# Kernel tuning notes

Measured on AMD Instinct MI355X. Metric: run time of the kernel, lower is better.

The kernel has to match this reference:

```python
import jax, jax.numpy as jnp
import numpy as np

N_NODES = 50000
N_EDGES = 1600000
IN_FEATS = 32
HIDDEN = 64
OUT_FEAT = 64


def setup_inputs() -> dict:
    key = jax.random.key(0)
    ks = jax.random.split(key, 8)
    inputs = jax.random.normal(ks[0], (N_NODES, IN_FEATS), dtype=jnp.float32)
    edge_weights = jax.random.uniform(ks[1], (N_EDGES, 1), dtype=jnp.float32)
    src = jax.random.randint(ks[2], (N_EDGES,), 0, N_NODES, dtype=jnp.int32)
    dst = jax.random.randint(ks[3], (N_EDGES,), 0, N_NODES, dtype=jnp.int32)
    W1 = jax.random.normal(ks[4], (IN_FEATS, HIDDEN), dtype=jnp.float32) / np.sqrt(IN_FEATS)
    b1 = jnp.zeros((HIDDEN,), dtype=jnp.float32)
    W2 = jax.random.normal(ks[5], (HIDDEN + IN_FEATS, OUT_FEAT), dtype=jnp.float32) / np.sqrt(HIDDEN + IN_FEATS)
    b2 = jnp.zeros((OUT_FEAT,), dtype=jnp.float32)
    return {"inputs": inputs, "edge_weights": edge_weights, "src": src, "dst": dst,
            "W1": W1, "b1": b1, "W2": W2, "b2": b2}


def _weighted_graph_conv(x, W, b, src, dst, ew, src_norm, dst_norm, n_nodes):
    # x: [N, Din] -> [N, Dout]
    x = x @ W                               # dense projection
    x = x * src_norm                        # D_out^{-1/2} scaling at source
    m = x[src] * ew                         # [E, Dout] gather * edge weight
    h = jax.ops.segment_sum(m, dst, num_segments=n_nodes)  # scatter-sum at dest
    return h * dst_norm + b                 # D_in^{-1/2} scaling + bias


def reference(inputs, edge_weights, src, dst, W1, b1, W2, b2):
    n = inputs.shape[0]
    ones = jnp.ones((src.shape[0],), dtype=jnp.float32)
    out_deg = jax.ops.segment_sum(ones, src, num_segments=n)
    in_deg = jax.ops.segment_sum(ones, dst, num_segments=n)
    src_norm = jnp.clip(out_deg, 1.0, None)[:, None] ** -0.5  # [N,1]
    dst_norm = jnp.clip(in_deg, 1.0, None)[:, None] ** -0.5   # [N,1]

    h = _weighted_graph_conv(inputs, W1, b1, src, dst, edge_weights, src_norm, dst_norm, n)
    h = jax.nn.relu(h)
    reminder = jnp.concatenate([h, inputs], axis=-1)  # re-inject input features
    h = _weighted_graph_conv(reminder, W2, b2, src, dst, edge_weights, src_norm, dst_norm, n)
    h = jax.nn.relu(h)
    # torch F.normalize(p=2, dim=-1, eps=1e-12)
    norm = jnp.linalg.norm(h, axis=-1, keepdims=True)
    return h / jnp.maximum(norm, 1e-12)
```

## Files before the change

### kernel.cpp

```cpp
#include <hip/hip_runtime.h>
#include <math.h>


#define BUK 128
#define BUK_SHIFT 7
#define FSH 256
#define SS 128
#define HIST_BS 512
#define NBUK_MAX 512
#define MAX_LDS_BYTES 131072
#define PNB 16

#define SCAN_BS 256
#define SCAN_ITEMS 4
#define SCAN_CHUNK (SCAN_BS * SCAN_ITEMS)

__device__ __forceinline__ unsigned short f2bf(float f) {
    unsigned u = __float_as_uint(f);
    return (unsigned short)((u + 0x7fffu + ((u >> 16) & 1u)) >> 16);
}
__device__ __forceinline__ float bf2f(unsigned short h) {
    return __uint_as_float((unsigned)h << 16);
}

__global__ void hist_src_kernel(const int* __restrict__ src, unsigned* __restrict__ partial_s,
                                int E, int NW4, int sliceS) {
    extern __shared__ unsigned h[];
    for (int i = threadIdx.x; i < NW4; i += blockDim.x) h[i] = 0u;
    __syncthreads();
    int s = blockIdx.x;
    int beg = s * sliceS, end = min(beg + sliceS, E);
    for (int e = beg + (int)threadIdx.x; e < end; e += blockDim.x) {
        int v = src[e];
        atomicAdd(&h[v >> 2], 1u << (8 * (v & 3)));
    }
    __syncthreads();
    unsigned* o = partial_s + (size_t)s * NW4;
    for (int i = threadIdx.x; i < NW4; i += blockDim.x) o[i] = h[i];
}

__global__ void reduce_src_kernel(const unsigned* __restrict__ partial_s,
                                  float* __restrict__ srcn, int N, int NW4) {
    int w = blockIdx.x * blockDim.x + threadIdx.x;
    if (w >= NW4) return;
    unsigned run = 0;
#pragma unroll 4
    for (int s = 0; s < SS; ++s) run += partial_s[(size_t)s * NW4 + w];
    int n0 = 4 * w;
#pragma unroll
    for (int k = 0; k < 4; ++k) {
        int n = n0 + k;
        if (n < N) srcn[n] = rsqrtf(fmaxf((float)((run >> (8 * k)) & 0xffu), 1.0f));
    }
}

__global__ void count_kernel(const int* __restrict__ dst, int* __restrict__ cntmat,
                             int E, int L, int NBUK) {
    __shared__ int c[NBUK_MAX];
    for (int i = threadIdx.x; i < NBUK; i += blockDim.x) c[i] = 0;
    __syncthreads();
    int s = blockIdx.x;
    int beg = s * L, end = min(beg + L, E);
    for (int e = beg + (int)threadIdx.x; e < end; e += blockDim.x)
        atomicAdd(&c[dst[e] >> BUK_SHIFT], 1);
    __syncthreads();
    for (int b = threadIdx.x; b < NBUK; b += blockDim.x)
        cntmat[(size_t)b * FSH + s] = c[b];
}

__global__ void scan_partial(const int* __restrict__ deg, int* __restrict__ bsum, int N) {
    __shared__ int sdata[SCAN_BS];
    int t = threadIdx.x;
    int base = blockIdx.x * SCAN_CHUNK + t * SCAN_ITEMS;
    int s = 0;
#pragma unroll
    for (int k = 0; k < SCAN_ITEMS; ++k) {
        int idx = base + k;
        s += (idx < N) ? deg[idx] : 0;
    }
    sdata[t] = s;
    __syncthreads();
    for (int off = SCAN_BS / 2; off > 0; off >>= 1) {
        if (t < off) sdata[t] += sdata[t + off];
        __syncthreads();
    }
    if (t == 0) bsum[blockIdx.x] = sdata[0];
}

__global__ void scan_bsums(int* __restrict__ bsum, int NB) {
    int carry = 0;
    for (int base = 0; base < NB; base += 64) {
        int l = base + (int)threadIdx.x;
        int v = (l < NB) ? bsum[l] : 0;
        int inc = v;
#pragma unroll
        for (int off = 1; off < 64; off <<= 1) {
            int tv = __shfl_up(inc, off, 64);
            if ((int)threadIdx.x >= off) inc += tv;
        }
        if (l < NB) bsum[l] = carry + inc - v;
        carry += __shfl(inc, 63, 64);
    }
}

__global__ void scan_final(const int* __restrict__ deg, const int* __restrict__ bsum,
                           int* __restrict__ offsets, int N) {
    __shared__ int sdata[SCAN_BS];
    int t = threadIdx.x;
    int base = blockIdx.x * SCAN_CHUNK + t * SCAN_ITEMS;
    int loc[SCAN_ITEMS];
    int s = 0;
#pragma unroll
    for (int k = 0; k < SCAN_ITEMS; ++k) {
        int idx = base + k;
        loc[k] = (idx < N) ? deg[idx] : 0;
        s += loc[k];
    }
    sdata[t] = s;
    __syncthreads();
    for (int off = 1; off < SCAN_BS; off <<= 1) {
        int v = (t >= off) ? sdata[t - off] : 0;
        __syncthreads();
        sdata[t] += v;
        __syncthreads();
    }
    int excl = sdata[t] - s + bsum[blockIdx.x];
#pragma unroll
    for (int k = 0; k < SCAN_ITEMS; ++k) {
        int idx = base + k;
        if (idx < N) {
            offsets[idx] = excl;
            if (idx == N - 1) offsets[N] = excl + loc[k];
        }
        excl += loc[k];
    }
}

__global__ void place_seg_kernel(const int* __restrict__ src, const int* __restrict__ dst,
                                 const float* __restrict__ ew, const int* __restrict__ cscan,
                                 uint2* __restrict__ inter, int E, int L, int NBUK) {
    __shared__ int cur[NBUK_MAX];
    int s = blockIdx.x;
    for (int b = threadIdx.x; b < NBUK; b += blockDim.x)
        cur[b] = cscan[(size_t)b * FSH + s];
    __syncthreads();
    int beg = s * L, end = min(beg + L, E);
    for (int e = beg + (int)threadIdx.x; e < end; e += blockDim.x) {
        int d = dst[e];
        int b = d >> BUK_SHIFT;
        int pos = atomicAdd(&cur[b], 1);
        inter[pos] = make_uint2((unsigned)src[e] | ((unsigned)f2bf(ew[e]) << 16),
                                (unsigned)(d & (BUK - 1)));
    }
}

__global__ void fill_final_kernel(const uint2* __restrict__ inter,
                                  const int* __restrict__ cscan,
                                  unsigned* __restrict__ edata, int* __restrict__ offsets,
                                  float* __restrict__ dstn, int N, int NBUK) {
    __shared__ int cnt[BUK];
    __shared__ int loff[BUK];
    int b = blockIdx.x;
    int t = threadIdx.x;
    int beg = cscan[(size_t)b * FSH];
    int end = cscan[(size_t)(b + 1) * FSH];
    if (t < BUK) cnt[t] = 0;
    __syncthreads();
    for (int p = beg + t; p < end; p += blockDim.x)
        atomicAdd(&cnt[inter[p].y], 1);
    __syncthreads();
    if (t < 64) {
        int carry = 0;
#pragma unroll
        for (int base = 0; base < BUK; base += 64) {
            int v = cnt[base + t];
            int inc = v;
#pragma unroll
            for (int off = 1; off < 64; off <<= 1) {
                int tv = __shfl_up(inc, off, 64);
                if (t >= off) inc += tv;
            }
            loff[base + t] = carry + inc - v;
            carry += __shfl(inc, 63, 64);
        }
    }
    __syncthreads();
    int node0 = b << BUK_SHIFT;
    if (t < BUK) {
        int n = node0 + t;
        if (n < N) {
            offsets[n] = beg + loff[t];
            dstn[n] = rsqrtf(fmaxf((float)cnt[t], 1.0f));
        }
    }
    if (b == NBUK - 1 && t == 0) offsets[N] = end;
    __syncthreads();
    if (t < BUK) cnt[t] = 0;
    __syncthreads();
    for (int p = beg + t; p < end; p += blockDim.x) {
        uint2 r = inter[p];
        int dl = (int)r.y;
        int rk = atomicAdd(&cnt[dl], 1);
        edata[beg + loff[dl] + rk] = r.x;
    }
}

__global__ void proj1_kernel(const float* __restrict__ X, const float* __restrict__ W1,
                             const float* __restrict__ srcn,
                             unsigned short* __restrict__ xp, int N) {
    __shared__ float w[32 * 64];
    __shared__ float xs[PNB][32];
    int tid = threadIdx.x;
    {
        const float4* Wv = (const float4*)W1;
        float4* wv = (float4*)w;
        for (int i = tid; i < 32 * 64 / 4; i += 256) wv[i] = Wv[i];
    }
    int nodeBase = blockIdx.x * PNB;
    int nrows = min(PNB, N - nodeBase);
    {
        const float4* Xv = (const float4*)(X + (size_t)nodeBase * 32);
        float4* xv = (float4*)&xs[0][0];
        for (int i = tid; i < nrows * 8; i += 256) xv[i] = Xv[i];
    }
    __syncthreads();
    int lane = tid & 63;
    int wid = tid >> 6;
    int m0 = wid * 4;
    float acc[4] = {0.f, 0.f, 0.f, 0.f};
#pragma unroll
    for (int kk = 0; kk < 32; kk += 4) {
        float w0 = w[(kk + 0) * 64 + lane], w1 = w[(kk + 1) * 64 + lane];
        float w2 = w[(kk + 2) * 64 + lane], w3 = w[(kk + 3) * 64 + lane];
#pragma unroll
        for (int m = 0; m < 4; ++m) {
            float4 x = *(const float4*)&xs[m0 + m][kk];
            acc[m] = fmaf(x.x, w0, fmaf(x.y, w1, fmaf(x.z, w2, fmaf(x.w, w3, acc[m]))));
        }
    }
#pragma unroll
    for (int m = 0; m < 4; ++m) {
        int n = nodeBase + m0 + m;
        if (n < N) xp[(size_t)n * 64 + lane] = f2bf(acc[m] * srcn[n]);
    }
}

__global__ void proj2_kernel(const float* __restrict__ h, const float* __restrict__ X,
                             const float* __restrict__ W2, const float* __restrict__ srcn,
                             unsigned short* __restrict__ xp, int N) {
    __shared__ float w[96 * 64];
    __shared__ float xs[PNB][96];
    int tid = threadIdx.x;
    {
        const float4* Wv = (const float4*)W2;
        float4* wv = (float4*)w;
        for (int i = tid; i < 96 * 64 / 4; i += 256) wv[i] = Wv[i];
    }
    int nodeBase = blockIdx.x * PNB;
    int nrows = min(PNB, N - nodeBase);
    for (int i = tid; i < nrows * 16; i += 256) {
        int r = i >> 4, c = i & 15;
        *(float4*)&xs[r][c * 4] = *(const float4*)(h + (size_t)(nodeBase + r) * 64 + c * 4);
    }
    for (int i = tid; i < nrows * 8; i += 256) {
        int r = i >> 3, c = i & 7;
        *(float4*)&xs[r][64 + c * 4] = *(const float4*)(X + (size_t)(nodeBase + r) * 32 + c * 4);
    }
    __syncthreads();
    int lane = tid & 63;
    int wid = tid >> 6;
    int m0 = wid * 4;
    float acc[4] = {0.f, 0.f, 0.f, 0.f};
#pragma unroll 6
    for (int kk = 0; kk < 96; kk += 4) {
        float w0 = w[(kk + 0) * 64 + lane], w1 = w[(kk + 1) * 64 + lane];
        float w2 = w[(kk + 2) * 64 + lane], w3 = w[(kk + 3) * 64 + lane];
#pragma unroll
        for (int m = 0; m < 4; ++m) {
            float4 x = *(const float4*)&xs[m0 + m][kk];
            acc[m] = fmaf(x.x, w0, fmaf(x.y, w1, fmaf(x.z, w2, fmaf(x.w, w3, acc[m]))));
        }
    }
#pragma unroll
    for (int m = 0; m < 4; ++m) {
        int n = nodeBase + m0 + m;
        if (n < N) xp[(size_t)n * 64 + lane] = f2bf(acc[m] * srcn[n]);
    }
}

template <bool FINAL>
__global__ void __launch_bounds__(256, 8)
gather_kernel(const int* __restrict__ offsets, const unsigned* __restrict__ edata,
              const unsigned short* __restrict__ xp, const float* __restrict__ dstn,
              const float* __restrict__ b, float* __restrict__ out, int N) {
    int lane = threadIdx.x & 63;
    int n = blockIdx.x * (blockDim.x >> 6) + (threadIdx.x >> 6);
    if (n >= N) return;
    int beg = offsets[n];
    int end = offsets[n + 1];
    float acc0 = 0.f, acc1 = 0.f, acc2 = 0.f, acc3 = 0.f;
    int p = beg;
    for (; p + 7 < end; p += 8) {
        unsigned e0 = edata[p],     e1 = edata[p + 1];
        unsigned e2 = edata[p + 2], e3 = edata[p + 3];
        unsigned e4 = edata[p + 4], e5 = edata[p + 5];
        unsigned e6 = edata[p + 6], e7 = edata[p + 7];
        float v0 = bf2f(xp[(size_t)(e0 & 0xffffu) * 64 + lane]);
        float v1 = bf2f(xp[(size_t)(e1 & 0xffffu) * 64 + lane]);
        float v2 = bf2f(xp[(size_t)(e2 & 0xffffu) * 64 + lane]);
        float v3 = bf2f(xp[(size_t)(e3 & 0xffffu) * 64 + lane]);
        float v4 = bf2f(xp[(size_t)(e4 & 0xffffu) * 64 + lane]);
        float v5 = bf2f(xp[(size_t)(e5 & 0xffffu) * 64 + lane]);
        float v6 = bf2f(xp[(size_t)(e6 & 0xffffu) * 64 + lane]);
        float v7 = bf2f(xp[(size_t)(e7 & 0xffffu) * 64 + lane]);
        acc0 = fmaf(v0, bf2f((unsigned short)(e0 >> 16)), acc0);
        acc1 = fmaf(v1, bf2f((unsigned short)(e1 >> 16)), acc1);
        acc2 = fmaf(v2, bf2f((unsigned short)(e2 >> 16)), acc2);
        acc3 = fmaf(v3, bf2f((unsigned short)(e3 >> 16)), acc3);
        acc0 = fmaf(v4, bf2f((unsigned short)(e4 >> 16)), acc0);
        acc1 = fmaf(v5, bf2f((unsigned short)(e5 >> 16)), acc1);
        acc2 = fmaf(v6, bf2f((unsigned short)(e6 >> 16)), acc2);
        acc3 = fmaf(v7, bf2f((unsigned short)(e7 >> 16)), acc3);
    }
    for (; p < end; ++p) {
        unsigned e0 = edata[p];
        acc0 = fmaf(bf2f(xp[(size_t)(e0 & 0xffffu) * 64 + lane]),
                    bf2f((unsigned short)(e0 >> 16)), acc0);
    }
    float v = fmaxf(((acc0 + acc1) + (acc2 + acc3)) * dstn[n] + b[lane], 0.0f);
    if (FINAL) {
        float s = v * v;
#pragma unroll
        for (int off = 32; off >= 1; off >>= 1) s += __shfl_xor(s, off, 64);
        v = v / fmaxf(sqrtf(s), 1e-12f);
    }
    out[(size_t)n * 64 + lane] = v;
}

__global__ void deg_kernel_i(const int* __restrict__ src, const int* __restrict__ dst,
                             int* __restrict__ degs, int* __restrict__ degd, int E) {
    int i = blockIdx.x * blockDim.x + threadIdx.x;
    if (i < E) {
        atomicAdd(&degs[src[i]], 1);
        atomicAdd(&degd[dst[i]], 1);
    }
}

__global__ void norm_kernel_i(const int* __restrict__ degs, const int* __restrict__ degd,
                              float* __restrict__ srcn, float* __restrict__ dstn, int N) {
    int i = blockIdx.x * blockDim.x + threadIdx.x;
    if (i < N) {
        srcn[i] = rsqrtf(fmaxf((float)degs[i], 1.0f));
        dstn[i] = rsqrtf(fmaxf((float)degd[i], 1.0f));
    }
}

__global__ void scatter_kernel(const int* __restrict__ src, const int* __restrict__ dst,
                               const float* __restrict__ ew,
                               const unsigned short* __restrict__ xp,
                               float* __restrict__ acc, int E) {
    int total = E * 64;
    int stride = gridDim.x * blockDim.x;
    for (int i = blockIdx.x * blockDim.x + threadIdx.x; i < total; i += stride) {
        int e = i >> 6;
        int f = i & 63;
        int s = src[e];
        int d = dst[e];
        float v = bf2f(xp[(size_t)s * 64 + f]) * ew[e];
        atomicAdd(&acc[(size_t)d * 64 + f], v);
    }
}

__global__ void relu_bias_kernel(float* __restrict__ h, const float* __restrict__ dstn,
                                 const float* __restrict__ b, int N) {
    int i = blockIdx.x * blockDim.x + threadIdx.x;
    if (i < N * 64) {
        int n = i >> 6;
        int j = i & 63;
        h[i] = fmaxf(h[i] * dstn[n] + b[j], 0.0f);
    }
}

__global__ void finalize_kernel(float* __restrict__ out, const float* __restrict__ dstn,
                                const float* __restrict__ b, int N) {
    int i = blockIdx.x * blockDim.x + threadIdx.x;
    int n = i >> 6;
    int f = i & 63;
    if (n >= N) return;
    float v = fmaxf(out[(size_t)n * 64 + f] * dstn[n] + b[f], 0.0f);
    float s = v * v;
#pragma unroll
    for (int off = 32; off >= 1; off >>= 1) s += __shfl_xor(s, off, 64);
    out[(size_t)n * 64 + f] = v / fmaxf(sqrtf(s), 1e-12f);
}


extern "C" void kernel_launch(void* const* d_in, const int* in_sizes, int n_in,
                              void* d_out, int out_size, void* d_ws, size_t ws_size,
                              hipStream_t stream) {
    const float* X   = (const float*)d_in[0];
    const float* ew  = (const float*)d_in[1];
    const int*   src = (const int*)d_in[2];
    const int*   dst = (const int*)d_in[3];
    const float* W1  = (const float*)d_in[4];
    const float* b1  = (const float*)d_in[5];
    const float* W2  = (const float*)d_in[6];
    const float* b2  = (const float*)d_in[7];

    const int N = in_sizes[0] / 32;
    const int E = in_sizes[2];
    const int NW4 = (N + 3) / 4;
    const int NBUK = (N + BUK - 1) / BUK;
    const int M = NBUK * FSH;
    const int L = (E + FSH - 1) / FSH;
    const int sliceS = (E + SS - 1) / SS;
    const int NBscan = (M + SCAN_CHUNK - 1) / SCAN_CHUNK;
    const int projGrid = (N + PNB - 1) / PNB;

    float* out = (float*)d_out;
    char* wsb = (char*)d_ws;

    size_t o = 0;
    auto alloc = [&](size_t bytes) { size_t p = o; o += (bytes + 255) & ~(size_t)255; return p; };
    size_t szPS = (size_t)SS * NW4 * 4;
    size_t szIN = (size_t)E * 8;
    size_t szXP = (size_t)N * 64 * 2;
    size_t szI = szPS > szIN ? szPS : szIN; if (szXP > szI) szI = szXP;
    size_t offI    = alloc(szI);
    size_t offEd   = alloc((size_t)E * 4);
    size_t offCS   = alloc(((size_t)M + 1) * 4);
    size_t offSrcn = alloc((size_t)N * 4);
    size_t offDstn = alloc((size_t)N * 4);
    size_t offOff  = alloc(((size_t)N + 1) * 4);
    size_t offBsum = alloc((size_t)NBscan * 4);
    size_t need = o;

    bool ok = (ws_size >= need) && (N <= 65536) && (NBUK <= NBUK_MAX) &&
              ((size_t)NW4 * 4 <= MAX_LDS_BYTES);

    if (ok) {
        unsigned*       partial_s = (unsigned*)(wsb + offI);
        uint2*          inter     = (uint2*)(wsb + offI);
        unsigned short* xp        = (unsigned short*)(wsb + offI);
        unsigned*       edata     = (unsigned*)(wsb + offEd);
        int*            cscan     = (int*)(wsb + offCS);
        float*          srcn      = (float*)(wsb + offSrcn);
        float*          dstn      = (float*)(wsb + offDstn);
        int*            offsets   = (int*)(wsb + offOff);
        int*            bsum      = (int*)(wsb + offBsum);

        hist_src_kernel<<<SS, HIST_BS, (size_t)NW4 * 4, stream>>>(src, partial_s, E, NW4, sliceS);
        reduce_src_kernel<<<(NW4 + 255) / 256, 256, 0, stream>>>(partial_s, srcn, N, NW4);

        count_kernel<<<FSH, HIST_BS, 0, stream>>>(dst, cscan, E, L, NBUK);
        scan_partial<<<NBscan, SCAN_BS, 0, stream>>>(cscan, bsum, M);
        scan_bsums<<<1, 64, 0, stream>>>(bsum, NBscan);
        scan_final<<<NBscan, SCAN_BS, 0, stream>>>(cscan, bsum, cscan, M);
        place_seg_kernel<<<FSH, HIST_BS, 0, stream>>>(src, dst, ew, cscan, inter, E, L, NBUK);
        fill_final_kernel<<<NBUK, 256, 0, stream>>>(inter, cscan, edata, offsets, dstn, N, NBUK);

        proj1_kernel<<<projGrid, 256, 0, stream>>>(X, W1, srcn, xp, N);
        gather_kernel<false><<<(N + 3) / 4, 256, 0, stream>>>(offsets, edata, xp, dstn, b1, out, N);
        proj2_kernel<<<projGrid, 256, 0, stream>>>(out, X, W2, srcn, xp, N);
        gather_kernel<true><<<(N + 3) / 4, 256, 0, stream>>>(offsets, edata, xp, dstn, b2, out, N);
    } else {
        float* ws   = (float*)d_ws;
        int*   degs = (int*)ws;
        int*   degd = (int*)(ws + N);
        float* srcn = ws + 2 * (size_t)N;
        float* dstn = ws + 3 * (size_t)N;
        unsigned short* xp = (unsigned short*)(ws + 4 * (size_t)N);

        hipMemsetAsync(degs, 0, 2 * (size_t)N * sizeof(float), stream);
        hipMemsetAsync(out, 0, (size_t)N * 64 * sizeof(float), stream);

        deg_kernel_i<<<(E + 255) / 256, 256, 0, stream>>>(src, dst, degs, degd, E);
        norm_kernel_i<<<(N + 255) / 256, 256, 0, stream>>>(degs, degd, srcn, dstn, N);

        proj1_kernel<<<projGrid, 256, 0, stream>>>(X, W1, srcn, xp, N);
        scatter_kernel<<<2048, 256, 0, stream>>>(src, dst, ew, xp, out, E);
        relu_bias_kernel<<<(N * 64 + 255) / 256, 256, 0, stream>>>(out, dstn, b1, N);

        proj2_kernel<<<projGrid, 256, 0, stream>>>(out, X, W2, srcn, xp, N);
        hipMemsetAsync(out, 0, (size_t)N * 64 * sizeof(float), stream);
        scatter_kernel<<<2048, 256, 0, stream>>>(src, dst, ew, xp, out, E);
        finalize_kernel<<<(N * 64 + 255) / 256, 256, 0, stream>>>(out, dstn, b2, N);
    }
}
```

Before: 222.9 us.

## Fuse layer-1 gather with layer-2 projection and batch edge loads via readlane

Replaces the layer-1 gather, its fp32 hidden-state write and the separate proj2 kernel with one kernel. It gathers a node's neighbours, applies bias and ReLU, and immediately projects through a bf16 copy of W2 held in shared memory. Edge records are now loaded 64 at a time with one coalesced load per wave and broadcast with readlane, instead of scalar loads per edge. The aim is to cut the hidden-state round trip through global memory and a kernel launch. In exchange, every block re-converts W2 into LDS, the per-node matvec runs serially over k with LDS broadcasts, and W2 is rounded to bf16, which adds precision error.

```diff
diff --git a/kernel.cpp b/kernel.cpp
--- a/kernel.cpp
+++ b/kernel.cpp
@@ -21,6 +21,52 @@
 }
 __device__ __forceinline__ float bf2f(unsigned short h) {
     return __uint_as_float((unsigned)h << 16);
+}
+
+__device__ __forceinline__ float edge_gather(const int* __restrict__ offsets,
+                                             const unsigned* __restrict__ edata,
+                                             const unsigned short* __restrict__ xp,
+                                             int n, int lane) {
+    int beg = offsets[n];
+    int end = offsets[n + 1];
+    float a0 = 0.f, a1 = 0.f, a2 = 0.f, a3 = 0.f;
+    for (int p = beg; p < end; p += 64) {
+        int cnt = min(64, end - p);
+        unsigned eb = (p + lane < end) ? edata[p + lane] : 0u;
+        int k = 0;
+        for (; k + 7 < cnt; k += 8) {
+            unsigned e0 = __builtin_amdgcn_readlane(eb, k);
+            unsigned e1 = __builtin_amdgcn_readlane(eb, k + 1);
+            unsigned e2 = __builtin_amdgcn_readlane(eb, k + 2);
+            unsigned e3 = __builtin_amdgcn_readlane(eb, k + 3);
+            unsigned e4 = __builtin_amdgcn_readlane(eb, k + 4);
+            unsigned e5 = __builtin_amdgcn_readlane(eb, k + 5);
+            unsigned e6 = __builtin_amdgcn_readlane(eb, k + 6);
+            unsigned e7 = __builtin_amdgcn_readlane(eb, k + 7);
+            float v0 = bf2f(xp[(size_t)(e0 & 0xffffu) * 64 + lane]);
+            float v1 = bf2f(xp[(size_t)(e1 & 0xffffu) * 64 + lane]);
+            float v2 = bf2f(xp[(size_t)(e2 & 0xffffu) * 64 + lane]);
+            float v3 = bf2f(xp[(size_t)(e3 & 0xffffu) * 64 + lane]);
+            float v4 = bf2f(xp[(size_t)(e4 & 0xffffu) * 64 + lane]);
+            float v5 = bf2f(xp[(size_t)(e5 & 0xffffu) * 64 + lane]);
+            float v6 = bf2f(xp[(size_t)(e6 & 0xffffu) * 64 + lane]);
+            float v7 = bf2f(xp[(size_t)(e7 & 0xffffu) * 64 + lane]);
+            a0 = fmaf(v0, bf2f((unsigned short)(e0 >> 16)), a0);
+            a1 = fmaf(v1, bf2f((unsigned short)(e1 >> 16)), a1);
+            a2 = fmaf(v2, bf2f((unsigned short)(e2 >> 16)), a2);
+            a3 = fmaf(v3, bf2f((unsigned short)(e3 >> 16)), a3);
+            a0 = fmaf(v4, bf2f((unsigned short)(e4 >> 16)), a0);
+            a1 = fmaf(v5, bf2f((unsigned short)(e5 >> 16)), a1);
+            a2 = fmaf(v6, bf2f((unsigned short)(e6 >> 16)), a2);
+            a3 = fmaf(v7, bf2f((unsigned short)(e7 >> 16)), a3);
+        }
+        for (; k < cnt; ++k) {
+            unsigned e0 = __builtin_amdgcn_readlane(eb, k);
+            a0 = fmaf(bf2f(xp[(size_t)(e0 & 0xffffu) * 64 + lane]),
+                      bf2f((unsigned short)(e0 >> 16)), a0);
+        }
+    }
+    return (a0 + a1) + (a2 + a3);
 }
 
 __global__ void hist_src_kernel(const int* __restrict__ src, unsigned* __restrict__ partial_s,
@@ -245,6 +291,72 @@
     }
 }
 
+__global__ void __launch_bounds__(256, 8)
+gp2_kernel(const int* __restrict__ offsets, const unsigned* __restrict__ edata,
+           const unsigned short* __restrict__ xp, const float* __restrict__ dstn,
+           const float* __restrict__ srcn, const float* __restrict__ b1,
+           const float* __restrict__ X, const float* __restrict__ W2,
+           unsigned short* __restrict__ xp2, int N) {
+    __shared__ unsigned short w2[96 * 64];
+    __shared__ float hrow[4][64];
+    __shared__ float xrow[4][32];
+    int tid = threadIdx.x;
+    for (int i = tid; i < 96 * 64; i += 256) w2[i] = f2bf(W2[i]);
+    __syncthreads();
+    int lane = tid & 63;
+    int wid = tid >> 6;
+    for (int j = 0; j < 4; ++j) {
+        int n = blockIdx.x * 16 + wid * 4 + j;
+        if (n >= N) return;
+        float acc = edge_gather(offsets, edata, xp, n, lane);
+        float h = fmaxf(acc * dstn[n] + b1[lane], 0.0f);
+        hrow[wid][lane] = h;
+        if (lane < 32) xrow[wid][lane] = X[(size_t)n * 32 + lane];
+        float p2 = 0.f;
+#pragma unroll 8
+        for (int k = 0; k < 64; ++k)
+            p2 = fmaf(hrow[wid][k], bf2f(w2[k * 64 + lane]), p2);
+#pragma unroll 8
+        for (int k = 0; k < 32; ++k)
+            p2 = fmaf(xrow[wid][k], bf2f(w2[(64 + k) * 64 + lane]), p2);
+        xp2[(size_t)n * 64 + lane] = f2bf(p2 * srcn[n]);
+    }
+}
+
+__global__ void __launch_bounds__(256, 8)
+gather_final_kernel(const int* __restrict__ offsets, const unsigned* __restrict__ edata,
+                    const unsigned short* __restrict__ xp2, const float* __restrict__ dstn,
+                    const float* __restrict__ b2, float* __restrict__ out, int N) {
+    int lane = threadIdx.x & 63;
+    int n = blockIdx.x * 4 + (threadIdx.x >> 6);
+    if (n >= N) return;
+    float acc = edge_gather(offsets, edata, xp2, n, lane);
+    float v = fmaxf(acc * dstn[n] + b2[lane], 0.0f);
+    float s = v * v;
+#pragma unroll
+    for (int off = 32; off >= 1; off >>= 1) s += __shfl_xor(s, off, 64);
+    v = v / fmaxf(sqrtf(s), 1e-12f);
+    out[(size_t)n * 64 + lane] = v;
+}
+
+__global__ void deg_kernel_i(const int* __restrict__ src, const int* __restrict__ dst,
+                             int* __restrict__ degs, int* __restrict__ degd, int E) {
+    int i = blockIdx.x * blockDim.x + threadIdx.x;
+    if (i < E) {
+        atomicAdd(&degs[src[i]], 1);
+        atomicAdd(&degd[dst[i]], 1);
+    }
+}
+
+__global__ void norm_kernel_i(const int* __restrict__ degs, const int* __restrict__ degd,
+                              float* __restrict__ srcn, float* __restrict__ dstn, int N) {
+    int i = blockIdx.x * blockDim.x + threadIdx.x;
+    if (i < N) {
+        srcn[i] = rsqrtf(fmaxf((float)degs[i], 1.0f));
+        dstn[i] = rsqrtf(fmaxf((float)degd[i], 1.0f));
+    }
+}
+
 __global__ void proj2_kernel(const float* __restrict__ h, const float* __restrict__ X,
                              const float* __restrict__ W2, const float* __restrict__ srcn,
                              unsigned short* __restrict__ xp, int N) {
@@ -285,73 +397,6 @@
     for (int m = 0; m < 4; ++m) {
         int n = nodeBase + m0 + m;
         if (n < N) xp[(size_t)n * 64 + lane] = f2bf(acc[m] * srcn[n]);
-    }
-}
-
-template <bool FINAL>
-__global__ void __launch_bounds__(256, 8)
-gather_kernel(const int* __restrict__ offsets, const unsigned* __restrict__ edata,
-              const unsigned short* __restrict__ xp, const float* __restrict__ dstn,
-              const float* __restrict__ b, float* __restrict__ out, int N) {
-    int lane = threadIdx.x & 63;
-    int n = blockIdx.x * (blockDim.x >> 6) + (threadIdx.x >> 6);
-    if (n >= N) return;
-    int beg = offsets[n];
-    int end = offsets[n + 1];
-    float acc0 = 0.f, acc1 = 0.f, acc2 = 0.f, acc3 = 0.f;
-    int p = beg;
-    for (; p + 7 < end; p += 8) {
-        unsigned e0 = edata[p],     e1 = edata[p + 1];
-        unsigned e2 = edata[p + 2], e3 = edata[p + 3];
-        unsigned e4 = edata[p + 4], e5 = edata[p + 5];
-        unsigned e6 = edata[p + 6], e7 = edata[p + 7];
-        float v0 = bf2f(xp[(size_t)(e0 & 0xffffu) * 64 + lane]);
-        float v1 = bf2f(xp[(size_t)(e1 & 0xffffu) * 64 + lane]);
-        float v2 = bf2f(xp[(size_t)(e2 & 0xffffu) * 64 + lane]);
-        float v3 = bf2f(xp[(size_t)(e3 & 0xffffu) * 64 + lane]);
-        float v4 = bf2f(xp[(size_t)(e4 & 0xffffu) * 64 + lane]);
-        float v5 = bf2f(xp[(size_t)(e5 & 0xffffu) * 64 + lane]);
-        float v6 = bf2f(xp[(size_t)(e6 & 0xffffu) * 64 + lane]);
-        float v7 = bf2f(xp[(size_t)(e7 & 0xffffu) * 64 + lane]);
-        acc0 = fmaf(v0, bf2f((unsigned short)(e0 >> 16)), acc0);
-        acc1 = fmaf(v1, bf2f((unsigned short)(e1 >> 16)), acc1);
-        acc2 = fmaf(v2, bf2f((unsigned short)(e2 >> 16)), acc2);
-        acc3 = fmaf(v3, bf2f((unsigned short)(e3 >> 16)), acc3);
-        acc0 = fmaf(v4, bf2f((unsigned short)(e4 >> 16)), acc0);
-        acc1 = fmaf(v5, bf2f((unsigned short)(e5 >> 16)), acc1);
-        acc2 = fmaf(v6, bf2f((unsigned short)(e6 >> 16)), acc2);
-        acc3 = fmaf(v7, bf2f((unsigned short)(e7 >> 16)), acc3);
-    }
-    for (; p < end; ++p) {
-        unsigned e0 = edata[p];
-        acc0 = fmaf(bf2f(xp[(size_t)(e0 & 0xffffu) * 64 + lane]),
-                    bf2f((unsigned short)(e0 >> 16)), acc0);
-    }
-    float v = fmaxf(((acc0 + acc1) + (acc2 + acc3)) * dstn[n] + b[lane], 0.0f);
-    if (FINAL) {
-        float s = v * v;
-#pragma unroll
-        for (int off = 32; off >= 1; off >>= 1) s += __shfl_xor(s, off, 64);
-        v = v / fmaxf(sqrtf(s), 1e-12f);
-    }
-    out[(size_t)n * 64 + lane] = v;
-}
-
-__global__ void deg_kernel_i(const int* __restrict__ src, const int* __restrict__ dst,
-                             int* __restrict__ degs, int* __restrict__ degd, int E) {
-    int i = blockIdx.x * blockDim.x + threadIdx.x;
-    if (i < E) {
-        atomicAdd(&degs[src[i]], 1);
-        atomicAdd(&degd[dst[i]], 1);
-    }
-}
-
-__global__ void norm_kernel_i(const int* __restrict__ degs, const int* __restrict__ degd,
-                              float* __restrict__ srcn, float* __restrict__ dstn, int N) {
-    int i = blockIdx.x * blockDim.x + threadIdx.x;
-    if (i < N) {
-        srcn[i] = rsqrtf(fmaxf((float)degs[i], 1.0f));
-        dstn[i] = rsqrtf(fmaxf((float)degd[i], 1.0f));
     }
 }
 
@@ -428,6 +473,7 @@
     size_t szI = szPS > szIN ? szPS : szIN; if (szXP > szI) szI = szXP;
     size_t offI    = alloc(szI);
     size_t offEd   = alloc((size_t)E * 4);
+    size_t offXP2  = alloc((size_t)N * 64 * 2);
     size_t offCS   = alloc(((size_t)M + 1) * 4);
     size_t offSrcn = alloc((size_t)N * 4);
     size_t offDstn = alloc((size_t)N * 4);
@@ -443,6 +489,7 @@
         uint2*          inter     = (uint2*)(wsb + offI);
         unsigned short* xp        = (unsigned short*)(wsb + offI);
         unsigned*       edata     = (unsigned*)(wsb + offEd);
+        unsigned short* xp2       = (unsigned short*)(wsb + offXP2);
         int*            cscan     = (int*)(wsb + offCS);
         float*          srcn      = (float*)(wsb + offSrcn);
         float*          dstn      = (float*)(wsb + offDstn);
@@ -460,9 +507,10 @@
         fill_final_kernel<<<NBUK, 256, 0, stream>>>(inter, cscan, edata, offsets, dstn, N, NBUK);
 
         proj1_kernel<<<projGrid, 256, 0, stream>>>(X, W1, srcn, xp, N);
-        gather_kernel<false><<<(N + 3) / 4, 256, 0, stream>>>(offsets, edata, xp, dstn, b1, out, N);
-        proj2_kernel<<<projGrid, 256, 0, stream>>>(out, X, W2, srcn, xp, N);
-        gather_kernel<true><<<(N + 3) / 4, 256, 0, stream>>>(offsets, edata, xp, dstn, b2, out, N);
+        gp2_kernel<<<(N + 15) / 16, 256, 0, stream>>>(offsets, edata, xp, dstn, srcn, b1,
+                                                      X, W2, xp2, N);
+        gather_final_kernel<<<(N + 3) / 4, 256, 0, stream>>>(offsets, edata, xp2, dstn,
+                                                             b2, out, N);
     } else {
         float* ws   = (float*)d_ws;
         int*   degs = (int*)ws;
```

After: 197.4 us. -11.5%, faster.
